# Kernel optimization log

Measured on AMD Instinct MI355X. Metric: run time of the kernel, lower is better.

## Reference

```python
import jax, jax.numpy as jnp
import numpy as np

NUM_GRAPHS = 131072
NUM_NODES = 25


def setup_inputs() -> dict:
    key = jax.random.key(0)
    k1, k2, k3 = jax.random.split(key, 3)
    G, N = NUM_GRAPHS, NUM_NODES
    x = jax.random.normal(k1, (G * N, 1), dtype=jnp.float32)
    # skeleton tree shared across graphs: root has parent -1, parent(i) = (i-1)//2
    p = np.empty(N, dtype=np.int64)
    p[0] = -1
    p[1:] = (np.arange(1, N) - 1) // 2
    parent = jnp.asarray(np.tile(p, G))
    offset = jax.random.normal(k2, (G * N, 6), dtype=jnp.float32)
    ax = jax.random.normal(k3, (N, 3), dtype=jnp.float32)  # per-node axes, shared across graphs
    axis = jnp.tile(ax, (G, 1))
    return {"x": x, "parent": parent, "offset": offset, "num_graphs": G, "axis": axis}


def _single_axis(e, axis_name):
    # e: [G, N] -> [G, N, 3, 3]
    c, s = jnp.cos(e), jnp.sin(e)
    z, o = jnp.zeros_like(c), jnp.ones_like(c)
    if axis_name == 'x':
        rows = [[o, z, z], [z, c, -s], [z, s, c]]
    elif axis_name == 'y':
        rows = [[c, z, s], [z, o, z], [-s, z, c]]
    else:  # 'z'
        rows = [[c, -s, z], [s, c, z], [z, z, o]]
    return jnp.stack([jnp.stack(r, axis=-1) for r in rows], axis=-2)


def _euler_xyz(rpy):
    # order 'xyz': Rz(rpy_z) @ Ry(rpy_y) @ Rx(rpy_x), matching transform_from_euler
    Rz = _single_axis(rpy[..., 2], 'z')
    Ry = _single_axis(rpy[..., 1], 'y')
    Rx = _single_axis(rpy[..., 0], 'x')
    return jnp.einsum('gnij,gnjk,gnkl->gnil', Rz, Ry, Rx)


def _rodrigues(theta, n):
    # theta: [G, N]; n: [N, 3] raw (unnormalized) axis, matching the original module
    c, s = jnp.cos(theta), jnp.sin(theta)
    v = 1.0 - c
    n1, n2, n3 = n[..., 0], n[..., 1], n[..., 2]
    rows = [
        [c + n1 * n1 * v, n1 * n2 * v - n3 * s, n1 * n3 * v + n2 * s],
        [n1 * n2 * v + n3 * s, c + n2 * n2 * v, n2 * n3 * v - n1 * s],
        [n1 * n3 * v - n2 * s, n2 * n3 * v + n1 * s, c + n3 * n3 * v],
    ]
    return jnp.stack([jnp.stack(r, axis=-1) for r in rows], axis=-2)


def _fk(x, offset, axis, parent_np, num_graphs):
    x = x.reshape(num_graphs, -1)          # [G, N]
    G, N = x.shape
    ax = axis.reshape(G, -1, 3)[0]          # [N, 3] (first graph only, like the original)
    theta = x * jnp.linalg.norm(ax, axis=-1)  # angle scaled by axis norm
    off = offset.reshape(G, -1, 6)
    xyz, rpy = off[..., :3], off[..., 3:]
    # per-node local rotation: rpy_transform @ axis_transform, [G, N, 3, 3]
    local = jnp.einsum('gnij,gnjk->gnik', _euler_xyz(rpy), _rodrigues(theta, ax))
    pos = [None] * N
    gpos = [None] * N
    rot = [None] * N
    for i in range(N):  # loop over fixed small skeleton (tree dependency)
        p = int(parent_np[i])
        if p == -1:
            pos[i] = jnp.zeros((G, 3), dtype=x.dtype)
            gpos[i] = xyz[:, i]
            rot[i] = local[:, i]
        else:
            d = jnp.einsum('gij,gj->gi', rot[p], xyz[:, i])
            pos[i] = d + pos[p]
            gpos[i] = d + gpos[p]
            rot[i] = jnp.einsum('gij,gjk->gik', rot[p], local[:, i])
    positions = jnp.stack(pos, axis=1).reshape(-1, 3)
    rot_matrices = jnp.stack(rot, axis=1).reshape(-1, 3, 3)
    global_positions = jnp.stack(gpos, axis=1).reshape(-1, 3)
    return positions, rot_matrices, global_positions


def reference(x, parent, offset, num_graphs, axis):
    parent_np = np.asarray(jax.device_get(parent)).reshape(num_graphs, -1)[0]
    return _fk(x, offset, axis, parent_np, num_graphs)
```

## Files before the change

### kernel.cpp

```cpp
#include <hip/hip_runtime.h>
#include <math.h>

#define NG 131072
#define NN 25
#define BT 128

__device__ __forceinline__ void mat3mul(const float* __restrict__ A,
                                        const float* __restrict__ B,
                                        float* __restrict__ C) {
#pragma unroll
    for (int i = 0; i < 3; ++i) {
#pragma unroll
        for (int j = 0; j < 3; ++j) {
            C[i * 3 + j] = A[i * 3 + 0] * B[0 + j]
                         + A[i * 3 + 1] * B[3 + j]
                         + A[i * 3 + 2] * B[6 + j];
        }
    }
}

__device__ __forceinline__ void local_rot(float roll, float pitch, float yaw,
                                          float theta, float a1, float a2, float a3,
                                          float* __restrict__ M) {
    float sx, cx, sy, cy, sz, cz, s, c;
    __sincosf(roll,  &sx, &cx);
    __sincosf(pitch, &sy, &cy);
    __sincosf(yaw,   &sz, &cz);
    __sincosf(theta, &s,  &c);
    float E[9];
    E[0] = cz * cy; E[1] = cz * sy * sx - sz * cx; E[2] = cz * sy * cx + sz * sx;
    E[3] = sz * cy; E[4] = sz * sy * sx + cz * cx; E[5] = sz * sy * cx - cz * sx;
    E[6] = -sy;     E[7] = cy * sx;                E[8] = cy * cx;
    const float v = 1.0f - c;
    float Q[9];
    Q[0] = c + a1 * a1 * v;  Q[1] = a1 * a2 * v - a3 * s;  Q[2] = a1 * a3 * v + a2 * s;
    Q[3] = a1 * a2 * v + a3 * s;  Q[4] = c + a2 * a2 * v;  Q[5] = a2 * a3 * v - a1 * s;
    Q[6] = a1 * a3 * v - a2 * s;  Q[7] = a2 * a3 * v + a1 * s;  Q[8] = c + a3 * a3 * v;
    mat3mul(E, Q, M);
}

__device__ __forceinline__ void leaf_rot_node(int n,
        const float* __restrict__ offg, const float* __restrict__ xg,
        const float* __restrict__ axis, float (*__restrict__ R)[9]) {
    const int p = (n - 1) >> 1;
    const float2 t23 = *(const float2*)(offg + n * 6 + 2);
    const float2 t45 = *(const float2*)(offg + n * 6 + 4);
    const float a1 = axis[n * 3 + 0];
    const float a2 = axis[n * 3 + 1];
    const float a3 = axis[n * 3 + 2];
    const float L = sqrtf(a1 * a1 + a2 * a2 + a3 * a3);
    const float theta = xg[n] * L;
    float M[9];
    local_rot(t23.y, t45.x, t45.y, theta, a1, a2, a3, M);
    mat3mul(R[p], M, R[n]);
}

__global__ __launch_bounds__(BT, 1)
void fk_kernel(const float* __restrict__ x,
               const float* __restrict__ offset,
               const float* __restrict__ axis,
               float* __restrict__ out)
{
    __shared__ __align__(16) float lds[BT * 78];

    const int tid = threadIdx.x;
    const long long blk = blockIdx.x;
    const long long g = blk * BT + tid;

    const float* __restrict__ xg   = x + g * NN;
    const float* __restrict__ offg = offset + g * (NN * 6);

    float* __restrict__ out_pos  = out;
    float* __restrict__ out_rot  = out + (long long)NG * NN * 3;
    float* __restrict__ out_gpos = out + (long long)NG * NN * 12;

    float R[NN][9];
    float rx = 0.f, ry = 0.f, rz = 0.f;

    float* lpos  = lds;
    float* lroot = lds + BT * 75;

#pragma unroll
    for (int n = 0; n < NN; ++n) {
        const int p = (n - 1) >> 1;
        const float2 t01 = *(const float2*)(offg + n * 6);
        const float2 t23 = *(const float2*)(offg + n * 6 + 2);

        float px, py, pz;
        if (n == 0) {
            rx = t01.x; ry = t01.y; rz = t23.x;
            px = 0.f; py = 0.f; pz = 0.f;
        } else {
            const float* pr = R[p];
            const float ppx = lpos[tid * 75 + p * 3 + 0];
            const float ppy = lpos[tid * 75 + p * 3 + 1];
            const float ppz = lpos[tid * 75 + p * 3 + 2];
            px = pr[0] * t01.x + pr[1] * t01.y + pr[2] * t23.x + ppx;
            py = pr[3] * t01.x + pr[4] * t01.y + pr[5] * t23.x + ppy;
            pz = pr[6] * t01.x + pr[7] * t01.y + pr[8] * t23.x + ppz;
        }
        lpos[tid * 75 + n * 3 + 0] = px;
        lpos[tid * 75 + n * 3 + 1] = py;
        lpos[tid * 75 + n * 3 + 2] = pz;

        if (n <= 11) {
            const float2 t45 = *(const float2*)(offg + n * 6 + 4);
            const float a1 = axis[n * 3 + 0];
            const float a2 = axis[n * 3 + 1];
            const float a3 = axis[n * 3 + 2];
            const float L = sqrtf(a1 * a1 + a2 * a2 + a3 * a3);
            const float theta = xg[n] * L;
            float M[9];
            local_rot(t23.y, t45.x, t45.y, theta, a1, a2, a3, M);
            if (n == 0) {
#pragma unroll
                for (int k = 0; k < 9; ++k) R[0][k] = M[k];
            } else {
                mat3mul(R[p], M, R[n]);
            }
        }
    }
    lroot[tid * 3 + 0] = rx;
    lroot[tid * 3 + 1] = ry;
    lroot[tid * 3 + 2] = rz;
    __syncthreads();

    {
        const float4* lp4 = (const float4*)lds;
        float4* dp = (float4*)(out_pos  + blk * (BT * 75));
        float4* dg = (float4*)(out_gpos + blk * (BT * 75));
        for (int i = tid; i < BT * 75 / 4; i += BT) {
            float4 v = lp4[i];
            dp[i] = v;
            const int b = 4 * i;
            float4 w;
            w.x = v.x + lroot[((b + 0) / 75) * 3 + ((b + 0) % 3)];
            w.y = v.y + lroot[((b + 1) / 75) * 3 + ((b + 1) % 3)];
            w.z = v.z + lroot[((b + 2) / 75) * 3 + ((b + 2) % 3)];
            w.w = v.w + lroot[((b + 3) / 75) * 3 + ((b + 3) % 3)];
            dg[i] = w;
        }
    }
    __syncthreads();

    float* __restrict__ dr = out_rot + blk * (long long)(BT * 225);

#pragma unroll
    for (int f = 0; f < 75; ++f) lds[tid * 75 + f] = R[f / 9][f % 9];
    __syncthreads();
    {
        for (int i = tid; i < BT * 75; i += BT) {
            const int q = i / 75;
            const int f = i - q * 75;
            dr[q * 225 + f] = lds[i];
        }
    }
    __syncthreads();

#pragma unroll
    for (int n = 12; n <= 16; ++n) leaf_rot_node(n, offg, xg, axis, R);
#pragma unroll
    for (int f = 0; f < 75; ++f) {
        const int F = 75 + f;
        lds[tid * 75 + f] = R[F / 9][F % 9];
    }
    __syncthreads();
    {
        for (int i = tid; i < BT * 75; i += BT) {
            const int q = i / 75;
            const int f = i - q * 75;
            dr[q * 225 + 75 + f] = lds[i];
        }
    }
    __syncthreads();

#pragma unroll
    for (int n = 17; n < NN; ++n) leaf_rot_node(n, offg, xg, axis, R);
#pragma unroll
    for (int f = 0; f < 75; ++f) {
        const int F = 150 + f;
        lds[tid * 75 + f] = R[F / 9][F % 9];
    }
    __syncthreads();
    {
        for (int i = tid; i < BT * 75; i += BT) {
            const int q = i / 75;
            const int f = i - q * 75;
            dr[q * 225 + 150 + f] = lds[i];
        }
    }
}

extern "C" void kernel_launch(void* const* d_in, const int* in_sizes, int n_in,
                              void* d_out, int out_size, void* d_ws, size_t ws_size,
                              hipStream_t stream) {
    const float* x      = (const float*)d_in[0];
    const float* offset = (const float*)d_in[2];
    const float* axis   = (const float*)d_in[4];
    float* out = (float*)d_out;

    fk_kernel<<<dim3(NG / BT), dim3(BT), 0, stream>>>(x, offset, axis, out);
}
```

Baseline: 341.5 us.

## Stage offset and x loads through LDS with coalesced, software-pipelined chunks

Each thread used to read its own graph's offsets and x with strided global loads. The block now loads them cooperatively and coalesced into LDS, in five chunks of five nodes, and prefetches the next chunk into registers while the current one is computed. Parent positions are kept in registers instead of being read back from LDS. The rotation write-out loops drop the per-iteration division for incremental index arithmetic. The cost is more LDS, extra barriers per chunk and higher register pressure from the prefetch buffer, while leaf nodes 12 to 24 still read offsets straight from global memory.

```diff
diff --git a/kernel.cpp b/kernel.cpp
--- a/kernel.cpp
+++ b/kernel.cpp
@@ -61,7 +61,10 @@
                const float* __restrict__ axis,
                float* __restrict__ out)
 {
-    __shared__ __align__(16) float lds[BT * 78];
+    __shared__ __align__(16) float s_pos[BT * 75];
+    __shared__ __align__(16) float s_root[BT * 3];
+    __shared__ __align__(16) float s_off[BT * 30];
+    __shared__ __align__(16) float s_x[BT * 13];
 
     const int tid = threadIdx.x;
     const long long blk = blockIdx.x;
@@ -74,59 +77,109 @@
     float* __restrict__ out_rot  = out + (long long)NG * NN * 3;
     float* __restrict__ out_gpos = out + (long long)NG * NN * 12;
 
+    const float2* __restrict__ ob = (const float2*)(offset) + blk * (BT * 75);
+    const float*  __restrict__ xb = x + blk * (BT * 25);
+
     float R[NN][9];
-    float rx = 0.f, ry = 0.f, rz = 0.f;
-
-    float* lpos  = lds;
-    float* lroot = lds + BT * 75;
-
-#pragma unroll
-    for (int n = 0; n < NN; ++n) {
-        const int p = (n - 1) >> 1;
-        const float2 t01 = *(const float2*)(offg + n * 6);
-        const float2 t23 = *(const float2*)(offg + n * 6 + 2);
-
-        float px, py, pz;
-        if (n == 0) {
-            rx = t01.x; ry = t01.y; rz = t23.x;
-            px = 0.f; py = 0.f; pz = 0.f;
-        } else {
-            const float* pr = R[p];
-            const float ppx = lpos[tid * 75 + p * 3 + 0];
-            const float ppy = lpos[tid * 75 + p * 3 + 1];
-            const float ppz = lpos[tid * 75 + p * 3 + 2];
-            px = pr[0] * t01.x + pr[1] * t01.y + pr[2] * t23.x + ppx;
-            py = pr[3] * t01.x + pr[4] * t01.y + pr[5] * t23.x + ppy;
-            pz = pr[6] * t01.x + pr[7] * t01.y + pr[8] * t23.x + ppz;
-        }
-        lpos[tid * 75 + n * 3 + 0] = px;
-        lpos[tid * 75 + n * 3 + 1] = py;
-        lpos[tid * 75 + n * 3 + 2] = pz;
-
-        if (n <= 11) {
-            const float2 t45 = *(const float2*)(offg + n * 6 + 4);
-            const float a1 = axis[n * 3 + 0];
-            const float a2 = axis[n * 3 + 1];
-            const float a3 = axis[n * 3 + 2];
-            const float L = sqrtf(a1 * a1 + a2 * a2 + a3 * a3);
-            const float theta = xg[n] * L;
-            float M[9];
-            local_rot(t23.y, t45.x, t45.y, theta, a1, a2, a3, M);
+    float pp[12][3];
+    float2 sv[15];
+
+    {
+        int q = tid / 12, r = tid - (tid / 12) * 12;
+#pragma unroll
+        for (int k = 0; k < 12; ++k) {
+            s_x[q * 13 + r] = xb[q * 25 + r];
+            q += 10; r += 8; if (r >= 12) { r -= 12; ++q; }
+        }
+    }
+    {
+        int q = tid / 15, r = tid - (tid / 15) * 15;
+#pragma unroll
+        for (int k = 0; k < 15; ++k) {
+            sv[k] = ob[q * 75 + r];
+            q += 8; r += 8; if (r >= 15) { r -= 15; ++q; }
+        }
+    }
+    {
+        float2* so = (float2*)s_off;
+        int q = tid / 15, r = tid - (tid / 15) * 15;
+#pragma unroll
+        for (int k = 0; k < 15; ++k) {
+            so[q * 15 + r] = sv[k];
+            q += 8; r += 8; if (r >= 15) { r -= 15; ++q; }
+        }
+    }
+    __syncthreads();
+
+#pragma unroll
+    for (int c = 0; c < 5; ++c) {
+        if (c < 4) {
+            int q = tid / 15, r = tid - (tid / 15) * 15;
+            const int base = (c + 1) * 15;
+#pragma unroll
+            for (int k = 0; k < 15; ++k) {
+                sv[k] = ob[q * 75 + base + r];
+                q += 8; r += 8; if (r >= 15) { r -= 15; ++q; }
+            }
+        }
+#pragma unroll
+        for (int j = 0; j < 5; ++j) {
+            const int n = c * 5 + j;
+            const int p = (n - 1) >> 1;
+            const float tx = s_off[tid * 30 + j * 6 + 0];
+            const float ty = s_off[tid * 30 + j * 6 + 1];
+            const float tz = s_off[tid * 30 + j * 6 + 2];
+            float px, py, pz;
             if (n == 0) {
-#pragma unroll
-                for (int k = 0; k < 9; ++k) R[0][k] = M[k];
+                s_root[tid * 3 + 0] = tx;
+                s_root[tid * 3 + 1] = ty;
+                s_root[tid * 3 + 2] = tz;
+                px = 0.f; py = 0.f; pz = 0.f;
             } else {
-                mat3mul(R[p], M, R[n]);
-            }
-        }
-    }
-    lroot[tid * 3 + 0] = rx;
-    lroot[tid * 3 + 1] = ry;
-    lroot[tid * 3 + 2] = rz;
-    __syncthreads();
-
-    {
-        const float4* lp4 = (const float4*)lds;
+                const float* pr = R[p];
+                px = pr[0] * tx + pr[1] * ty + pr[2] * tz + pp[p][0];
+                py = pr[3] * tx + pr[4] * ty + pr[5] * tz + pp[p][1];
+                pz = pr[6] * tx + pr[7] * ty + pr[8] * tz + pp[p][2];
+            }
+            if (n < 12) { pp[n][0] = px; pp[n][1] = py; pp[n][2] = pz; }
+            s_pos[tid * 75 + n * 3 + 0] = px;
+            s_pos[tid * 75 + n * 3 + 1] = py;
+            s_pos[tid * 75 + n * 3 + 2] = pz;
+
+            if (n <= 11) {
+                const float roll  = s_off[tid * 30 + j * 6 + 3];
+                const float pitch = s_off[tid * 30 + j * 6 + 4];
+                const float yaw   = s_off[tid * 30 + j * 6 + 5];
+                const float a1 = axis[n * 3 + 0];
+                const float a2 = axis[n * 3 + 1];
+                const float a3 = axis[n * 3 + 2];
+                const float L = sqrtf(a1 * a1 + a2 * a2 + a3 * a3);
+                const float theta = s_x[tid * 13 + n] * L;
+                float M[9];
+                local_rot(roll, pitch, yaw, theta, a1, a2, a3, M);
+                if (n == 0) {
+#pragma unroll
+                    for (int k = 0; k < 9; ++k) R[0][k] = M[k];
+                } else {
+                    mat3mul(R[p], M, R[n]);
+                }
+            }
+        }
+        __syncthreads();
+        if (c < 4) {
+            float2* so = (float2*)s_off;
+            int q = tid / 15, r = tid - (tid / 15) * 15;
+#pragma unroll
+            for (int k = 0; k < 15; ++k) {
+                so[q * 15 + r] = sv[k];
+                q += 8; r += 8; if (r >= 15) { r -= 15; ++q; }
+            }
+            __syncthreads();
+        }
+    }
+
+    {
+        const float4* lp4 = (const float4*)s_pos;
         float4* dp = (float4*)(out_pos  + blk * (BT * 75));
         float4* dg = (float4*)(out_gpos + blk * (BT * 75));
         for (int i = tid; i < BT * 75 / 4; i += BT) {
@@ -134,10 +187,10 @@
             dp[i] = v;
             const int b = 4 * i;
             float4 w;
-            w.x = v.x + lroot[((b + 0) / 75) * 3 + ((b + 0) % 3)];
-            w.y = v.y + lroot[((b + 1) / 75) * 3 + ((b + 1) % 3)];
-            w.z = v.z + lroot[((b + 2) / 75) * 3 + ((b + 2) % 3)];
-            w.w = v.w + lroot[((b + 3) / 75) * 3 + ((b + 3) % 3)];
+            w.x = v.x + s_root[((b + 0) / 75) * 3 + ((b + 0) % 3)];
+            w.y = v.y + s_root[((b + 1) / 75) * 3 + ((b + 1) % 3)];
+            w.z = v.z + s_root[((b + 2) / 75) * 3 + ((b + 2) % 3)];
+            w.w = v.w + s_root[((b + 3) / 75) * 3 + ((b + 3) % 3)];
             dg[i] = w;
         }
     }
@@ -146,13 +199,13 @@
     float* __restrict__ dr = out_rot + blk * (long long)(BT * 225);
 
 #pragma unroll
-    for (int f = 0; f < 75; ++f) lds[tid * 75 + f] = R[f / 9][f % 9];
-    __syncthreads();
-    {
-        for (int i = tid; i < BT * 75; i += BT) {
-            const int q = i / 75;
-            const int f = i - q * 75;
-            dr[q * 225 + f] = lds[i];
+    for (int f = 0; f < 75; ++f) s_pos[tid * 75 + f] = R[f / 9][f % 9];
+    __syncthreads();
+    {
+        int q = tid / 75, f = tid - (tid / 75) * 75;
+        for (int it = 0; it < 75; ++it) {
+            dr[q * 225 + f] = s_pos[q * 75 + f];
+            ++q; f += 53; if (f >= 75) { f -= 75; ++q; }
         }
     }
     __syncthreads();
@@ -162,14 +215,14 @@
 #pragma unroll
     for (int f = 0; f < 75; ++f) {
         const int F = 75 + f;
-        lds[tid * 75 + f] = R[F / 9][F % 9];
-    }
-    __syncthreads();
-    {
-        for (int i = tid; i < BT * 75; i += BT) {
-            const int q = i / 75;
-            const int f = i - q * 75;
-            dr[q * 225 + 75 + f] = lds[i];
+        s_pos[tid * 75 + f] = R[F / 9][F % 9];
+    }
+    __syncthreads();
+    {
+        int q = tid / 75, f = tid - (tid / 75) * 75;
+        for (int it = 0; it < 75; ++it) {
+            dr[q * 225 + 75 + f] = s_pos[q * 75 + f];
+            ++q; f += 53; if (f >= 75) { f -= 75; ++q; }
         }
     }
     __syncthreads();
@@ -179,14 +232,14 @@
 #pragma unroll
     for (int f = 0; f < 75; ++f) {
         const int F = 150 + f;
-        lds[tid * 75 + f] = R[F / 9][F % 9];
-    }
-    __syncthreads();
-    {
-        for (int i = tid; i < BT * 75; i += BT) {
-            const int q = i / 75;
-            const int f = i - q * 75;
-            dr[q * 225 + 150 + f] = lds[i];
+        s_pos[tid * 75 + f] = R[F / 9][F % 9];
+    }
+    __syncthreads();
+    {
+        int q = tid / 75, f = tid - (tid / 75) * 75;
+        for (int it = 0; it < 75; ++it) {
+            dr[q * 225 + 150 + f] = s_pos[q * 75 + f];
+            ++q; f += 53; if (f >= 75) { f -= 75; ++q; }
         }
     }
 }
```

Measured after the change: 337.6 us. About the same (-1.1%).
